# Kernel tuning notes

Measured on AMD Instinct MI355X. Metric: run time of the kernel, lower is better.

The kernel has to match this reference:

```python
import jax, jax.numpy as jnp
import numpy as np

B, C, N = 8, 768, 256
H = 12            # num_heads[0]
D = C // H        # head_dim = 64


def setup_inputs() -> dict:
    key = jax.random.key(0)
    ks = jax.random.split(key, 4)
    s = 0.02
    return {
        "x_ori": jax.random.normal(ks[0], (B, C, N), jnp.float32),
        "cross": jax.random.normal(ks[1], (B, C, N), jnp.float32),
        "W_proj": jax.random.normal(ks[2], (C, C), jnp.float32) * s,
        "b_proj": jnp.zeros((C,), jnp.float32),
        "W_dep": jax.random.normal(ks[3], (C, C), jnp.float32) * s,
        "b_dep": jnp.zeros((C,), jnp.float32),
    }


def reference(x_ori, cross, W_proj, b_proj, W_dep, b_dep):
    # x_ori, cross: [B, C, N] with channel axis factored as (head_dim D, num_heads H)
    Bn, Cn, Nn = x_ori.shape
    Nc = cross.shape[-1]
    scale = D ** (-0.5)

    # 'B (d H) N -> B d (H N)'
    x = x_ori.reshape(Bn, D, H, Nn).reshape(Bn, D, H * Nn)

    # proj over channel axis (1x1 conv): [B, C, Nc]
    cp = jnp.einsum('oc,bcn->bon', W_proj, cross) + b_proj[None, :, None]
    cp = cp.reshape(Bn, D, H, Nc).reshape(Bn, D, H * Nc)      # 'B (d H) Nc -> B d (H Nc)'

    # 'B (d H) Nc -> B (H Nc) d'
    cr = cross.reshape(Bn, D, H, Nc).transpose(0, 2, 3, 1).reshape(Bn, H * Nc, D)

    # raw attention (no softmax in original source)
    atten = jnp.einsum('bdm,bdn->bmn', x, cp) * scale          # [B, H*N, H*Nc]
    out = jnp.einsum('bmn,bnd->bmd', atten, cr)                # [B, H*N, D]

    # 'B (N H) d -> B N (H d)'  (note (num, head) grouping per source)
    out = out.reshape(Bn, Nn, H, D).reshape(Bn, Nn, H * D)

    y = out @ W_dep.T + b_dep                                  # deproj: [B, N, C]
    # skip connection (dropout is identity at eval / drop_ratio=0)
    return x_ori + y.transpose(0, 2, 1)
```

## Files before the change

### kernel.cpp

```cpp
#include <hip/hip_runtime.h>

typedef unsigned short u16;
typedef short bf16x8 __attribute__((ext_vector_type(8)));
typedef float f32x4 __attribute__((ext_vector_type(4)));

#define BB 8
#define CC 768
#define NN 256
#define HH 12
#define DD 64
#define K3 3072
#define BCN 196608
#define SCALE 0.125f
#define LDP 72

__device__ __forceinline__ u16 f2b(float f) {
    union { float f; unsigned int i; } v; v.f = f;
    unsigned int r = v.i + 0x7FFFu + ((v.i >> 16) & 1u);
    return (u16)(r >> 16);
}

__global__ __launch_bounds__(256) void k_prep(
    const float* __restrict__ x, const float* __restrict__ cross, u16* __restrict__ outw)
{
    const int n0 = blockIdx.x * 64;
    const int b  = blockIdx.z;
    const int t  = threadIdx.x;
    __shared__ float T[64][68];
    u16* crT = outw;
    u16* xT  = outw + (size_t)BB * BCN;
    if (blockIdx.y < HH) {
        const int h = blockIdx.y;
        const float* xb = x + b * BCN;
        {
            const int d = t >> 2, fq = t & 3;
            const float* src = xb + (d * HH + h) * NN + n0;
            #pragma unroll
            for (int j = 0; j < 4; ++j) {
                const int nl = (fq + 4 * j) * 4;
                float4 v = *reinterpret_cast<const float4*>(src + nl);
                T[d][nl + 0] = v.x; T[d][nl + 1] = v.y; T[d][nl + 2] = v.z; T[d][nl + 3] = v.w;
            }
        }
        __syncthreads();
        {
            const int nn = t >> 2, dq = t & 3;
            u16* dst = xT + b * BCN + (h * NN + n0 + nn) * DD;
            #pragma unroll
            for (int j = 0; j < 4; ++j) {
                const int d0 = (dq + 4 * j) * 4;
                ushort4 w;
                w.x = f2b(T[d0 + 0][nn]); w.y = f2b(T[d0 + 1][nn]);
                w.z = f2b(T[d0 + 2][nn]); w.w = f2b(T[d0 + 3][nn]);
                *reinterpret_cast<ushort4*>(dst + d0) = w;
            }
        }
    } else {
        const int c0 = (blockIdx.y - HH) * 64;
        const float* crb = cross + b * BCN;
        {
            const int r = t >> 2, fq = t & 3;
            const float* src = crb + (c0 + r) * NN + n0;
            #pragma unroll
            for (int j = 0; j < 4; ++j) {
                const int nl = (fq + 4 * j) * 4;
                float4 v = *reinterpret_cast<const float4*>(src + nl);
                T[r][nl + 0] = v.x; T[r][nl + 1] = v.y; T[r][nl + 2] = v.z; T[r][nl + 3] = v.w;
            }
        }
        __syncthreads();
        {
            const int nn = t >> 2, cq = t & 3;
            u16* dst = crT + b * BCN + (n0 + nn) * CC + c0;
            #pragma unroll
            for (int j = 0; j < 4; ++j) {
                const int cl = (cq + 4 * j) * 4;
                ushort4 w;
                w.x = f2b(T[cl + 0][nn]); w.y = f2b(T[cl + 1][nn]);
                w.z = f2b(T[cl + 2][nn]); w.w = f2b(T[cl + 3][nn]);
                *reinterpret_cast<ushort4*>(dst + cl) = w;
            }
        }
    }
}

__global__ __launch_bounds__(256) void k_proj(
    const float* __restrict__ Wp, const u16* __restrict__ crT_all,
    const float* __restrict__ bp, u16* __restrict__ cp)
{
    const int n0 = blockIdx.x * 64;
    const int o0 = blockIdx.y * 64;
    const int b  = blockIdx.z;
    __shared__ __align__(16) u16 As[64 * LDP];
    __shared__ __align__(16) u16 Bs[64 * LDP];
    const int t = threadIdx.x;
    const int lane = t & 63, wave = t >> 6;
    const int q = lane >> 4, tx = lane & 15;
    const int wm = (wave & 1) * 32, wn = (wave >> 1) * 32;
    const u16* crT = crT_all + b * BCN;
    f32x4 acc[2][2] = {};
    for (int c0 = 0; c0 < CC; c0 += 64) {
        {
            const int r = t >> 2, cq = t & 3;
            const float* src = Wp + (o0 + r) * CC + c0;
            u16* dst = As + r * LDP;
            #pragma unroll
            for (int j = 0; j < 4; ++j) {
                const int cl = (cq + 4 * j) * 4;
                float4 v = *reinterpret_cast<const float4*>(src + cl);
                ushort4 w; w.x = f2b(v.x); w.y = f2b(v.y); w.z = f2b(v.z); w.w = f2b(v.w);
                *reinterpret_cast<ushort4*>(dst + cl) = w;
            }
        }
        {
            const int r = t >> 3, ch = (t & 7) * 8;
            *reinterpret_cast<uint4*>(Bs + r * LDP + ch) =
                *reinterpret_cast<const uint4*>(crT + (n0 + r) * CC + c0 + ch);
            *reinterpret_cast<uint4*>(Bs + (r + 32) * LDP + ch) =
                *reinterpret_cast<const uint4*>(crT + (n0 + r + 32) * CC + c0 + ch);
        }
        __syncthreads();
        #pragma unroll
        for (int kk = 0; kk < 2; ++kk) {
            bf16x8 a0 = *reinterpret_cast<bf16x8*>(As + (wm + tx) * LDP + kk * 32 + q * 8);
            bf16x8 a1 = *reinterpret_cast<bf16x8*>(As + (wm + 16 + tx) * LDP + kk * 32 + q * 8);
            bf16x8 b0 = *reinterpret_cast<bf16x8*>(Bs + (wn + tx) * LDP + kk * 32 + q * 8);
            bf16x8 b1 = *reinterpret_cast<bf16x8*>(Bs + (wn + 16 + tx) * LDP + kk * 32 + q * 8);
            acc[0][0] = __builtin_amdgcn_mfma_f32_16x16x32_bf16(a0, b0, acc[0][0], 0, 0, 0);
            acc[0][1] = __builtin_amdgcn_mfma_f32_16x16x32_bf16(a0, b1, acc[0][1], 0, 0, 0);
            acc[1][0] = __builtin_amdgcn_mfma_f32_16x16x32_bf16(a1, b0, acc[1][0], 0, 0, 0);
            acc[1][1] = __builtin_amdgcn_mfma_f32_16x16x32_bf16(a1, b1, acc[1][1], 0, 0, 0);
        }
        __syncthreads();
    }
    u16* cpb = cp + b * BCN;
    #pragma unroll
    for (int i = 0; i < 2; ++i)
        #pragma unroll
        for (int j = 0; j < 2; ++j)
            #pragma unroll
            for (int r = 0; r < 4; ++r) {
                const int o = o0 + wm + i * 16 + q * 4 + r;
                const int n = n0 + wn + j * 16 + tx;
                cpb[o * NN + n] = f2b(acc[i][j][r] + bp[o]);
            }
}

__global__ __launch_bounds__(256) void k_gram(
    const float* __restrict__ cross, const u16* __restrict__ cp, float* __restrict__ G)
{
    const int kb = blockIdx.x * 64;
    const int b  = blockIdx.y;
    __shared__ __align__(16) u16 As[64 * LDP];
    __shared__ __align__(16) u16 Bs[64 * LDP];
    const int t = threadIdx.x;
    const int lane = t & 63, wave = t >> 6;
    const int q = lane >> 4, tx = lane & 15;
    const int wm = (wave & 1) * 32, wn = (wave >> 1) * 32;
    const float* crb = cross + b * BCN;
    const u16* cpb = cp + b * BCN;
    f32x4 acc[2][2] = {};
    {
        const int r = t >> 2, cq = t & 3;
        const float* src = crb + r * K3 + kb;
        u16* dst = As + r * LDP;
        #pragma unroll
        for (int j = 0; j < 4; ++j) {
            const int cl = (cq + 4 * j) * 4;
            float4 v = *reinterpret_cast<const float4*>(src + cl);
            ushort4 w; w.x = f2b(v.x); w.y = f2b(v.y); w.z = f2b(v.z); w.w = f2b(v.w);
            *reinterpret_cast<ushort4*>(dst + cl) = w;
        }
    }
    {
        const int r = t >> 3, ch = (t & 7) * 8;
        *reinterpret_cast<uint4*>(Bs + r * LDP + ch) =
            *reinterpret_cast<const uint4*>(cpb + r * K3 + kb + ch);
        *reinterpret_cast<uint4*>(Bs + (r + 32) * LDP + ch) =
            *reinterpret_cast<const uint4*>(cpb + (r + 32) * K3 + kb + ch);
    }
    __syncthreads();
    #pragma unroll
    for (int kk = 0; kk < 2; ++kk) {
        bf16x8 a0 = *reinterpret_cast<bf16x8*>(As + (wm + tx) * LDP + kk * 32 + q * 8);
        bf16x8 a1 = *reinterpret_cast<bf16x8*>(As + (wm + 16 + tx) * LDP + kk * 32 + q * 8);
        bf16x8 b0 = *reinterpret_cast<bf16x8*>(Bs + (wn + tx) * LDP + kk * 32 + q * 8);
        bf16x8 b1 = *reinterpret_cast<bf16x8*>(Bs + (wn + 16 + tx) * LDP + kk * 32 + q * 8);
        acc[0][0] = __builtin_amdgcn_mfma_f32_16x16x32_bf16(a0, b0, acc[0][0], 0, 0, 0);
        acc[0][1] = __builtin_amdgcn_mfma_f32_16x16x32_bf16(a0, b1, acc[0][1], 0, 0, 0);
        acc[1][0] = __builtin_amdgcn_mfma_f32_16x16x32_bf16(a1, b0, acc[1][0], 0, 0, 0);
        acc[1][1] = __builtin_amdgcn_mfma_f32_16x16x32_bf16(a1, b1, acc[1][1], 0, 0, 0);
    }
    float* Gb = G + b * 4096;
    #pragma unroll
    for (int i = 0; i < 2; ++i)
        #pragma unroll
        for (int j = 0; j < 2; ++j)
            #pragma unroll
            for (int r = 0; r < 4; ++r) {
                const int dd = wm + i * 16 + q * 4 + r;
                const int d  = wn + j * 16 + tx;
                atomicAdd(Gb + dd * DD + d, acc[i][j][r] * SCALE);
            }
}

__global__ __launch_bounds__(256) void k_xm(
    const u16* __restrict__ xT_all, const float* __restrict__ G, u16* __restrict__ U)
{
    const int m0 = blockIdx.x * 64;
    const int b  = blockIdx.y;
    __shared__ __align__(16) u16 As[64 * LDP];
    __shared__ __align__(16) u16 Bs[64 * LDP];
    const int t = threadIdx.x;
    const int lane = t & 63, wave = t >> 6;
    const int q = lane >> 4, tx = lane & 15;
    const int wm = (wave & 1) * 32, wn = (wave >> 1) * 32;
    const u16* xT = xT_all + b * BCN;
    const float* Gb = G + b * 4096;
    f32x4 acc[2][2] = {};
    {
        const int r = t >> 3, ch = (t & 7) * 8;
        *reinterpret_cast<uint4*>(As + r * LDP + ch) =
            *reinterpret_cast<const uint4*>(xT + (m0 + r) * DD + ch);
        *reinterpret_cast<uint4*>(As + (r + 32) * LDP + ch) =
            *reinterpret_cast<const uint4*>(xT + (m0 + r + 32) * DD + ch);
    }
    {
        const int r = t >> 2, cq = t & 3;
        const float* src = Gb + r * DD;
        u16* dst = Bs + r * LDP;
        #pragma unroll
        for (int j = 0; j < 4; ++j) {
            const int cl = (cq + 4 * j) * 4;
            float4 v = *reinterpret_cast<const float4*>(src + cl);
            ushort4 w; w.x = f2b(v.x); w.y = f2b(v.y); w.z = f2b(v.z); w.w = f2b(v.w);
            *reinterpret_cast<ushort4*>(dst + cl) = w;
        }
    }
    __syncthreads();
    #pragma unroll
    for (int kk = 0; kk < 2; ++kk) {
        bf16x8 a0 = *reinterpret_cast<bf16x8*>(As + (wm + tx) * LDP + kk * 32 + q * 8);
        bf16x8 a1 = *reinterpret_cast<bf16x8*>(As + (wm + 16 + tx) * LDP + kk * 32 + q * 8);
        bf16x8 b0 = *reinterpret_cast<bf16x8*>(Bs + (wn + tx) * LDP + kk * 32 + q * 8);
        bf16x8 b1 = *reinterpret_cast<bf16x8*>(Bs + (wn + 16 + tx) * LDP + kk * 32 + q * 8);
        acc[0][0] = __builtin_amdgcn_mfma_f32_16x16x32_bf16(a0, b0, acc[0][0], 0, 0, 0);
        acc[0][1] = __builtin_amdgcn_mfma_f32_16x16x32_bf16(a0, b1, acc[0][1], 0, 0, 0);
        acc[1][0] = __builtin_amdgcn_mfma_f32_16x16x32_bf16(a1, b0, acc[1][0], 0, 0, 0);
        acc[1][1] = __builtin_amdgcn_mfma_f32_16x16x32_bf16(a1, b1, acc[1][1], 0, 0, 0);
    }
    u16* Ub = U + b * BCN;
    #pragma unroll
    for (int i = 0; i < 2; ++i)
        #pragma unroll
        for (int j = 0; j < 2; ++j)
            #pragma unroll
            for (int r = 0; r < 4; ++r) {
                const int m  = m0 + wm + i * 16 + q * 4 + r;
                const int dd = wn + j * 16 + tx;
                Ub[m * DD + dd] = f2b(acc[i][j][r]);
            }
}

__global__ __launch_bounds__(256) void k_dep(
    const float* __restrict__ Wd, const u16* __restrict__ U,
    const float* __restrict__ bd, const float* __restrict__ x, float* __restrict__ out)
{
    const int n0 = blockIdx.x * 64;
    const int o0 = blockIdx.y * 64;
    const int b  = blockIdx.z;
    __shared__ __align__(16) u16 As[64 * LDP];
    __shared__ __align__(16) u16 Bs[64 * LDP];
    const int t = threadIdx.x;
    const int lane = t & 63, wave = t >> 6;
    const int q = lane >> 4, tx = lane & 15;
    const int wm = (wave & 1) * 32, wn = (wave >> 1) * 32;
    const u16* Ub = U + b * BCN;
    f32x4 acc[2][2] = {};
    for (int c0 = 0; c0 < CC; c0 += 64) {
        {
            const int r = t >> 2, cq = t & 3;
            const float* src = Wd + (o0 + r) * CC + c0;
            u16* dst = As + r * LDP;
            #pragma unroll
            for (int j = 0; j < 4; ++j) {
                const int cl = (cq + 4 * j) * 4;
                float4 v = *reinterpret_cast<const float4*>(src + cl);
                ushort4 w; w.x = f2b(v.x); w.y = f2b(v.y); w.z = f2b(v.z); w.w = f2b(v.w);
                *reinterpret_cast<ushort4*>(dst + cl) = w;
            }
        }
        {
            const int r = t >> 3, ch = (t & 7) * 8;
            *reinterpret_cast<uint4*>(Bs + r * LDP + ch) =
                *reinterpret_cast<const uint4*>(Ub + (n0 + r) * CC + c0 + ch);
            *reinterpret_cast<uint4*>(Bs + (r + 32) * LDP + ch) =
                *reinterpret_cast<const uint4*>(Ub + (n0 + r + 32) * CC + c0 + ch);
        }
        __syncthreads();
        #pragma unroll
        for (int kk = 0; kk < 2; ++kk) {
            bf16x8 a0 = *reinterpret_cast<bf16x8*>(As + (wm + tx) * LDP + kk * 32 + q * 8);
            bf16x8 a1 = *reinterpret_cast<bf16x8*>(As + (wm + 16 + tx) * LDP + kk * 32 + q * 8);
            bf16x8 b0 = *reinterpret_cast<bf16x8*>(Bs + (wn + tx) * LDP + kk * 32 + q * 8);
            bf16x8 b1 = *reinterpret_cast<bf16x8*>(Bs + (wn + 16 + tx) * LDP + kk * 32 + q * 8);
            acc[0][0] = __builtin_amdgcn_mfma_f32_16x16x32_bf16(a0, b0, acc[0][0], 0, 0, 0);
            acc[0][1] = __builtin_amdgcn_mfma_f32_16x16x32_bf16(a0, b1, acc[0][1], 0, 0, 0);
            acc[1][0] = __builtin_amdgcn_mfma_f32_16x16x32_bf16(a1, b0, acc[1][0], 0, 0, 0);
            acc[1][1] = __builtin_amdgcn_mfma_f32_16x16x32_bf16(a1, b1, acc[1][1], 0, 0, 0);
        }
        __syncthreads();
    }
    #pragma unroll
    for (int i = 0; i < 2; ++i)
        #pragma unroll
        for (int j = 0; j < 2; ++j)
            #pragma unroll
            for (int r = 0; r < 4; ++r) {
                const int o = o0 + wm + i * 16 + q * 4 + r;
                const int n = n0 + wn + j * 16 + tx;
                const int idx = b * BCN + o * NN + n;
                out[idx] = acc[i][j][r] + bd[o] + x[idx];
            }
}

extern "C" void kernel_launch(void* const* d_in, const int* in_sizes, int n_in,
                              void* d_out, int out_size, void* d_ws, size_t ws_size,
                              hipStream_t stream) {
    const float* x_ori = (const float*)d_in[0];
    const float* cross = (const float*)d_in[1];
    const float* Wp    = (const float*)d_in[2];
    const float* bp    = (const float*)d_in[3];
    const float* Wd    = (const float*)d_in[4];
    const float* bd    = (const float*)d_in[5];
    float* out = (float*)d_out;

    u16*   cp = (u16*)d_ws;
    u16*   U  = (u16*)d_ws;
    float* G  = (float*)((char*)d_ws + (size_t)BB * BCN * sizeof(u16));
    u16*   prep = (u16*)d_out;
    const u16* crT = prep;
    const u16* xT  = prep + (size_t)BB * BCN;

    hipMemsetAsync(G, 0, (size_t)BB * DD * DD * sizeof(float), stream);
    k_prep<<<dim3(4, 24, BB), 256, 0, stream>>>(x_ori, cross, prep);
    k_proj<<<dim3(4, 12, BB), 256, 0, stream>>>(Wp, crT, bp, cp);
    k_gram<<<dim3(48, BB), 256, 0, stream>>>(cross, cp, G);
    k_xm  <<<dim3(48, BB), 256, 0, stream>>>(xT, G, U);
    k_dep <<<dim3(4, 12, BB), 256, 0, stream>>>(Wd, U, bd, x_ori, out);
}
```

Baseline: 132.9 us.

## Fuse all stages into one cooperative persistent kernel with grid syncs

```diff
diff --git a/kernel.cpp b/kernel.cpp
--- a/kernel.cpp
+++ b/kernel.cpp
@@ -1,4 +1,7 @@
 #include <hip/hip_runtime.h>
+#include <hip/hip_cooperative_groups.h>
+
+namespace cg = cooperative_groups;
 
 typedef unsigned short u16;
 typedef short bf16x8 __attribute__((ext_vector_type(8)));
@@ -13,6 +16,7 @@
 #define BCN 196608
 #define SCALE 0.125f
 #define LDP 72
+#define NBLK 384
 
 __device__ __forceinline__ u16 f2b(float f) {
     union { float f; unsigned int i; } v; v.f = f;
@@ -20,93 +24,171 @@
     return (u16)(r >> 16);
 }
 
-__global__ __launch_bounds__(256) void k_prep(
-    const float* __restrict__ x, const float* __restrict__ cross, u16* __restrict__ outw)
+__global__ __launch_bounds__(256) void k_fused(
+    const float* __restrict__ x, const float* __restrict__ cross,
+    const float* __restrict__ Wp, const float* __restrict__ bp,
+    const float* __restrict__ Wd, const float* __restrict__ bd,
+    char* outbase, char* ws)
 {
-    const int n0 = blockIdx.x * 64;
-    const int b  = blockIdx.z;
-    const int t  = threadIdx.x;
-    __shared__ float T[64][68];
-    u16* crT = outw;
-    u16* xT  = outw + (size_t)BB * BCN;
-    if (blockIdx.y < HH) {
-        const int h = blockIdx.y;
-        const float* xb = x + b * BCN;
-        {
-            const int d = t >> 2, fq = t & 3;
-            const float* src = xb + (d * HH + h) * NN + n0;
-            #pragma unroll
-            for (int j = 0; j < 4; ++j) {
-                const int nl = (fq + 4 * j) * 4;
-                float4 v = *reinterpret_cast<const float4*>(src + nl);
-                T[d][nl + 0] = v.x; T[d][nl + 1] = v.y; T[d][nl + 2] = v.z; T[d][nl + 3] = v.w;
-            }
-        }
-        __syncthreads();
-        {
-            const int nn = t >> 2, dq = t & 3;
-            u16* dst = xT + b * BCN + (h * NN + n0 + nn) * DD;
-            #pragma unroll
-            for (int j = 0; j < 4; ++j) {
-                const int d0 = (dq + 4 * j) * 4;
-                ushort4 w;
-                w.x = f2b(T[d0 + 0][nn]); w.y = f2b(T[d0 + 1][nn]);
-                w.z = f2b(T[d0 + 2][nn]); w.w = f2b(T[d0 + 3][nn]);
-                *reinterpret_cast<ushort4*>(dst + d0) = w;
-            }
-        }
-    } else {
-        const int c0 = (blockIdx.y - HH) * 64;
-        const float* crb = cross + b * BCN;
-        {
-            const int r = t >> 2, fq = t & 3;
-            const float* src = crb + (c0 + r) * NN + n0;
-            #pragma unroll
-            for (int j = 0; j < 4; ++j) {
-                const int nl = (fq + 4 * j) * 4;
-                float4 v = *reinterpret_cast<const float4*>(src + nl);
-                T[r][nl + 0] = v.x; T[r][nl + 1] = v.y; T[r][nl + 2] = v.z; T[r][nl + 3] = v.w;
-            }
-        }
-        __syncthreads();
-        {
-            const int nn = t >> 2, cq = t & 3;
-            u16* dst = crT + b * BCN + (n0 + nn) * CC + c0;
-            #pragma unroll
-            for (int j = 0; j < 4; ++j) {
-                const int cl = (cq + 4 * j) * 4;
-                ushort4 w;
-                w.x = f2b(T[cl + 0][nn]); w.y = f2b(T[cl + 1][nn]);
-                w.z = f2b(T[cl + 2][nn]); w.w = f2b(T[cl + 3][nn]);
-                *reinterpret_cast<ushort4*>(dst + cl) = w;
-            }
-        }
-    }
-}
-
-__global__ __launch_bounds__(256) void k_proj(
-    const float* __restrict__ Wp, const u16* __restrict__ crT_all,
-    const float* __restrict__ bp, u16* __restrict__ cp)
-{
-    const int n0 = blockIdx.x * 64;
-    const int o0 = blockIdx.y * 64;
-    const int b  = blockIdx.z;
-    __shared__ __align__(16) u16 As[64 * LDP];
-    __shared__ __align__(16) u16 Bs[64 * LDP];
+    __shared__ __align__(16) u16 SMEM[2 * 64 * LDP];
+    u16* As = SMEM;
+    u16* Bs = SMEM + 64 * LDP;
+    float (*T)[68] = reinterpret_cast<float(*)[68]>(SMEM);
+
+    float* out = (float*)outbase;
+    u16*   crT = (u16*)outbase;
+    u16*   xT  = crT + (size_t)BB * BCN;
+    u16*   cp  = (u16*)ws;
+    u16*   U   = cp;
+    float* G   = (float*)(ws + (size_t)BB * BCN * sizeof(u16));
+
+    const int blk = blockIdx.x;
     const int t = threadIdx.x;
     const int lane = t & 63, wave = t >> 6;
     const int q = lane >> 4, tx = lane & 15;
     const int wm = (wave & 1) * 32, wn = (wave >> 1) * 32;
-    const u16* crT = crT_all + b * BCN;
-    f32x4 acc[2][2] = {};
-    for (int c0 = 0; c0 < CC; c0 += 64) {
+    cg::grid_group grid = cg::this_grid();
+
+    if (blk < BB) {
+        float* Gb = G + blk * 4096;
+        #pragma unroll
+        for (int j = 0; j < 4; ++j) {
+            float4 z = {0.f, 0.f, 0.f, 0.f};
+            *reinterpret_cast<float4*>(Gb + (t * 4 + j * 1024)) = z;
+        }
+    }
+    #pragma unroll
+    for (int jj = 0; jj < 2; ++jj) {
+        const int j  = blk * 2 + jj;
+        const int n0 = (j & 3) * 64;
+        const int yy = (j >> 2) % 24;
+        const int b  = j / 96;
+        if (yy < HH) {
+            const int h = yy;
+            const float* xb = x + b * BCN;
+            {
+                const int d = t >> 2, fq = t & 3;
+                const float* src = xb + (d * HH + h) * NN + n0;
+                #pragma unroll
+                for (int u = 0; u < 4; ++u) {
+                    const int nl = (fq + 4 * u) * 4;
+                    float4 v = *reinterpret_cast<const float4*>(src + nl);
+                    T[d][nl + 0] = v.x; T[d][nl + 1] = v.y; T[d][nl + 2] = v.z; T[d][nl + 3] = v.w;
+                }
+            }
+            __syncthreads();
+            {
+                const int nn = t >> 2, dq = t & 3;
+                u16* dst = xT + b * BCN + (h * NN + n0 + nn) * DD;
+                #pragma unroll
+                for (int u = 0; u < 4; ++u) {
+                    const int d0 = (dq + 4 * u) * 4;
+                    ushort4 w;
+                    w.x = f2b(T[d0 + 0][nn]); w.y = f2b(T[d0 + 1][nn]);
+                    w.z = f2b(T[d0 + 2][nn]); w.w = f2b(T[d0 + 3][nn]);
+                    *reinterpret_cast<ushort4*>(dst + d0) = w;
+                }
+            }
+        } else {
+            const int c0 = (yy - HH) * 64;
+            const float* crb = cross + b * BCN;
+            {
+                const int r = t >> 2, fq = t & 3;
+                const float* src = crb + (c0 + r) * NN + n0;
+                #pragma unroll
+                for (int u = 0; u < 4; ++u) {
+                    const int nl = (fq + 4 * u) * 4;
+                    float4 v = *reinterpret_cast<const float4*>(src + nl);
+                    T[r][nl + 0] = v.x; T[r][nl + 1] = v.y; T[r][nl + 2] = v.z; T[r][nl + 3] = v.w;
+                }
+            }
+            __syncthreads();
+            {
+                const int nn = t >> 2, cq = t & 3;
+                u16* dst = crT + b * BCN + (n0 + nn) * CC + c0;
+                #pragma unroll
+                for (int u = 0; u < 4; ++u) {
+                    const int cl = (cq + 4 * u) * 4;
+                    ushort4 w;
+                    w.x = f2b(T[cl + 0][nn]); w.y = f2b(T[cl + 1][nn]);
+                    w.z = f2b(T[cl + 2][nn]); w.w = f2b(T[cl + 3][nn]);
+                    *reinterpret_cast<ushort4*>(dst + cl) = w;
+                }
+            }
+        }
+        __syncthreads();
+    }
+
+    grid.sync();
+
+    {
+        const int n0 = (blk & 3) * 64;
+        const int o0 = ((blk >> 2) % 12) * 64;
+        const int b  = blk / 48;
+        const u16* crTb = crT + b * BCN;
+        f32x4 acc[2][2] = {};
+        for (int c0 = 0; c0 < CC; c0 += 64) {
+            {
+                const int r = t >> 2, cq = t & 3;
+                const float* src = Wp + (o0 + r) * CC + c0;
+                u16* dst = As + r * LDP;
+                #pragma unroll
+                for (int u = 0; u < 4; ++u) {
+                    const int cl = (cq + 4 * u) * 4;
+                    float4 v = *reinterpret_cast<const float4*>(src + cl);
+                    ushort4 w; w.x = f2b(v.x); w.y = f2b(v.y); w.z = f2b(v.z); w.w = f2b(v.w);
+                    *reinterpret_cast<ushort4*>(dst + cl) = w;
+                }
+            }
+            {
+                const int r = t >> 3, ch = (t & 7) * 8;
+                *reinterpret_cast<uint4*>(Bs + r * LDP + ch) =
+                    *reinterpret_cast<const uint4*>(crTb + (n0 + r) * CC + c0 + ch);
+                *reinterpret_cast<uint4*>(Bs + (r + 32) * LDP + ch) =
+                    *reinterpret_cast<const uint4*>(crTb + (n0 + r + 32) * CC + c0 + ch);
+            }
+            __syncthreads();
+            #pragma unroll
+            for (int kk = 0; kk < 2; ++kk) {
+                bf16x8 a0 = *reinterpret_cast<bf16x8*>(As + (wm + tx) * LDP + kk * 32 + q * 8);
+                bf16x8 a1 = *reinterpret_cast<bf16x8*>(As + (wm + 16 + tx) * LDP + kk * 32 + q * 8);
+                bf16x8 b0 = *reinterpret_cast<bf16x8*>(Bs + (wn + tx) * LDP + kk * 32 + q * 8);
+                bf16x8 b1 = *reinterpret_cast<bf16x8*>(Bs + (wn + 16 + tx) * LDP + kk * 32 + q * 8);
+                acc[0][0] = __builtin_amdgcn_mfma_f32_16x16x32_bf16(a0, b0, acc[0][0], 0, 0, 0);
+                acc[0][1] = __builtin_amdgcn_mfma_f32_16x16x32_bf16(a0, b1, acc[0][1], 0, 0, 0);
+                acc[1][0] = __builtin_amdgcn_mfma_f32_16x16x32_bf16(a1, b0, acc[1][0], 0, 0, 0);
+                acc[1][1] = __builtin_amdgcn_mfma_f32_16x16x32_bf16(a1, b1, acc[1][1], 0, 0, 0);
+            }
+            __syncthreads();
+        }
+        u16* cpb = cp + b * BCN;
+        #pragma unroll
+        for (int i = 0; i < 2; ++i)
+            #pragma unroll
+            for (int j2 = 0; j2 < 2; ++j2)
+                #pragma unroll
+                for (int r = 0; r < 4; ++r) {
+                    const int o = o0 + wm + i * 16 + q * 4 + r;
+                    const int n = n0 + wn + j2 * 16 + tx;
+                    cpb[o * NN + n] = f2b(acc[i][j2][r] + bp[o]);
+                }
+    }
+
+    grid.sync();
+
+    {
+        const int kb = (blk % 48) * 64;
+        const int b  = blk / 48;
+        const float* crb = cross + b * BCN;
+        const u16* cpb = cp + b * BCN;
+        f32x4 acc[2][2] = {};
         {
             const int r = t >> 2, cq = t & 3;
-            const float* src = Wp + (o0 + r) * CC + c0;
+            const float* src = crb + r * K3 + kb;
             u16* dst = As + r * LDP;
             #pragma unroll
-            for (int j = 0; j < 4; ++j) {
-                const int cl = (cq + 4 * j) * 4;
+            for (int u = 0; u < 4; ++u) {
+                const int cl = (cq + 4 * u) * 4;
                 float4 v = *reinterpret_cast<const float4*>(src + cl);
                 ushort4 w; w.x = f2b(v.x); w.y = f2b(v.y); w.z = f2b(v.z); w.w = f2b(v.w);
                 *reinterpret_cast<ushort4*>(dst + cl) = w;
@@ -115,9 +197,9 @@
         {
             const int r = t >> 3, ch = (t & 7) * 8;
             *reinterpret_cast<uint4*>(Bs + r * LDP + ch) =
-                *reinterpret_cast<const uint4*>(crT + (n0 + r) * CC + c0 + ch);
+                *reinterpret_cast<const uint4*>(cpb + r * K3 + kb + ch);
             *reinterpret_cast<uint4*>(Bs + (r + 32) * LDP + ch) =
-                *reinterpret_cast<const uint4*>(crT + (n0 + r + 32) * CC + c0 + ch);
+                *reinterpret_cast<const uint4*>(cpb + (r + 32) * K3 + kb + ch);
         }
         __syncthreads();
         #pragma unroll
@@ -132,170 +214,45 @@
             acc[1][1] = __builtin_amdgcn_mfma_f32_16x16x32_bf16(a1, b1, acc[1][1], 0, 0, 0);
         }
         __syncthreads();
-    }
-    u16* cpb = cp + b * BCN;
-    #pragma unroll
-    for (int i = 0; i < 2; ++i)
-        #pragma unroll
-        for (int j = 0; j < 2; ++j)
-            #pragma unroll
-            for (int r = 0; r < 4; ++r) {
-                const int o = o0 + wm + i * 16 + q * 4 + r;
-                const int n = n0 + wn + j * 16 + tx;
-                cpb[o * NN + n] = f2b(acc[i][j][r] + bp[o]);
-            }
-}
-
-__global__ __launch_bounds__(256) void k_gram(
-    const float* __restrict__ cross, const u16* __restrict__ cp, float* __restrict__ G)
-{
-    const int kb = blockIdx.x * 64;
-    const int b  = blockIdx.y;
-    __shared__ __align__(16) u16 As[64 * LDP];
-    __shared__ __align__(16) u16 Bs[64 * LDP];
-    const int t = threadIdx.x;
-    const int lane = t & 63, wave = t >> 6;
-    const int q = lane >> 4, tx = lane & 15;
-    const int wm = (wave & 1) * 32, wn = (wave >> 1) * 32;
-    const float* crb = cross + b * BCN;
-    const u16* cpb = cp + b * BCN;
-    f32x4 acc[2][2] = {};
+        float* Gb = G + b * 4096;
+        #pragma unroll
+        for (int i = 0; i < 2; ++i)
+            #pragma unroll
+            for (int j2 = 0; j2 < 2; ++j2)
+                #pragma unroll
+                for (int r = 0; r < 4; ++r) {
+                    const int dd = wm + i * 16 + q * 4 + r;
+                    const int d  = wn + j2 * 16 + tx;
+                    atomicAdd(Gb + dd * DD + d, acc[i][j2][r] * SCALE);
+                }
+    }
+
+    grid.sync();
+
     {
-        const int r = t >> 2, cq = t & 3;
-        const float* src = crb + r * K3 + kb;
-        u16* dst = As + r * LDP;
-        #pragma unroll
-        for (int j = 0; j < 4; ++j) {
-            const int cl = (cq + 4 * j) * 4;
-            float4 v = *reinterpret_cast<const float4*>(src + cl);
-            ushort4 w; w.x = f2b(v.x); w.y = f2b(v.y); w.z = f2b(v.z); w.w = f2b(v.w);
-            *reinterpret_cast<ushort4*>(dst + cl) = w;
-        }
-    }
-    {
-        const int r = t >> 3, ch = (t & 7) * 8;
-        *reinterpret_cast<uint4*>(Bs + r * LDP + ch) =
-            *reinterpret_cast<const uint4*>(cpb + r * K3 + kb + ch);
-        *reinterpret_cast<uint4*>(Bs + (r + 32) * LDP + ch) =
-            *reinterpret_cast<const uint4*>(cpb + (r + 32) * K3 + kb + ch);
-    }
-    __syncthreads();
-    #pragma unroll
-    for (int kk = 0; kk < 2; ++kk) {
-        bf16x8 a0 = *reinterpret_cast<bf16x8*>(As + (wm + tx) * LDP + kk * 32 + q * 8);
-        bf16x8 a1 = *reinterpret_cast<bf16x8*>(As + (wm + 16 + tx) * LDP + kk * 32 + q * 8);
-        bf16x8 b0 = *reinterpret_cast<bf16x8*>(Bs + (wn + tx) * LDP + kk * 32 + q * 8);
-        bf16x8 b1 = *reinterpret_cast<bf16x8*>(Bs + (wn + 16 + tx) * LDP + kk * 32 + q * 8);
-        acc[0][0] = __builtin_amdgcn_mfma_f32_16x16x32_bf16(a0, b0, acc[0][0], 0, 0, 0);
-        acc[0][1] = __builtin_amdgcn_mfma_f32_16x16x32_bf16(a0, b1, acc[0][1], 0, 0, 0);
-        acc[1][0] = __builtin_amdgcn_mfma_f32_16x16x32_bf16(a1, b0, acc[1][0], 0, 0, 0);
-        acc[1][1] = __builtin_amdgcn_mfma_f32_16x16x32_bf16(a1, b1, acc[1][1], 0, 0, 0);
-    }
-    float* Gb = G + b * 4096;
-    #pragma unroll
-    for (int i = 0; i < 2; ++i)
-        #pragma unroll
-        for (int j = 0; j < 2; ++j)
-            #pragma unroll
-            for (int r = 0; r < 4; ++r) {
-                const int dd = wm + i * 16 + q * 4 + r;
-                const int d  = wn + j * 16 + tx;
-                atomicAdd(Gb + dd * DD + d, acc[i][j][r] * SCALE);
-            }
-}
-
-__global__ __launch_bounds__(256) void k_xm(
-    const u16* __restrict__ xT_all, const float* __restrict__ G, u16* __restrict__ U)
-{
-    const int m0 = blockIdx.x * 64;
-    const int b  = blockIdx.y;
-    __shared__ __align__(16) u16 As[64 * LDP];
-    __shared__ __align__(16) u16 Bs[64 * LDP];
-    const int t = threadIdx.x;
-    const int lane = t & 63, wave = t >> 6;
-    const int q = lane >> 4, tx = lane & 15;
-    const int wm = (wave & 1) * 32, wn = (wave >> 1) * 32;
-    const u16* xT = xT_all + b * BCN;
-    const float* Gb = G + b * 4096;
-    f32x4 acc[2][2] = {};
-    {
-        const int r = t >> 3, ch = (t & 7) * 8;
-        *reinterpret_cast<uint4*>(As + r * LDP + ch) =
-            *reinterpret_cast<const uint4*>(xT + (m0 + r) * DD + ch);
-        *reinterpret_cast<uint4*>(As + (r + 32) * LDP + ch) =
-            *reinterpret_cast<const uint4*>(xT + (m0 + r + 32) * DD + ch);
-    }
-    {
-        const int r = t >> 2, cq = t & 3;
-        const float* src = Gb + r * DD;
-        u16* dst = Bs + r * LDP;
-        #pragma unroll
-        for (int j = 0; j < 4; ++j) {
-            const int cl = (cq + 4 * j) * 4;
-            float4 v = *reinterpret_cast<const float4*>(src + cl);
-            ushort4 w; w.x = f2b(v.x); w.y = f2b(v.y); w.z = f2b(v.z); w.w = f2b(v.w);
-            *reinterpret_cast<ushort4*>(dst + cl) = w;
-        }
-    }
-    __syncthreads();
-    #pragma unroll
-    for (int kk = 0; kk < 2; ++kk) {
-        bf16x8 a0 = *reinterpret_cast<bf16x8*>(As + (wm + tx) * LDP + kk * 32 + q * 8);
-        bf16x8 a1 = *reinterpret_cast<bf16x8*>(As + (wm + 16 + tx) * LDP + kk * 32 + q * 8);
-        bf16x8 b0 = *reinterpret_cast<bf16x8*>(Bs + (wn + tx) * LDP + kk * 32 + q * 8);
-        bf16x8 b1 = *reinterpret_cast<bf16x8*>(Bs + (wn + 16 + tx) * LDP + kk * 32 + q * 8);
-        acc[0][0] = __builtin_amdgcn_mfma_f32_16x16x32_bf16(a0, b0, acc[0][0], 0, 0, 0);
-        acc[0][1] = __builtin_amdgcn_mfma_f32_16x16x32_bf16(a0, b1, acc[0][1], 0, 0, 0);
-        acc[1][0] = __builtin_amdgcn_mfma_f32_16x16x32_bf16(a1, b0, acc[1][0], 0, 0, 0);
-        acc[1][1] = __builtin_amdgcn_mfma_f32_16x16x32_bf16(a1, b1, acc[1][1], 0, 0, 0);
-    }
-    u16* Ub = U + b * BCN;
-    #pragma unroll
-    for (int i = 0; i < 2; ++i)
-        #pragma unroll
-        for (int j = 0; j < 2; ++j)
-            #pragma unroll
-            for (int r = 0; r < 4; ++r) {
-                const int m  = m0 + wm + i * 16 + q * 4 + r;
-                const int dd = wn + j * 16 + tx;
-                Ub[m * DD + dd] = f2b(acc[i][j][r]);
-            }
-}
-
-__global__ __launch_bounds__(256) void k_dep(
-    const float* __restrict__ Wd, const u16* __restrict__ U,
-    const float* __restrict__ bd, const float* __restrict__ x, float* __restrict__ out)
-{
-    const int n0 = blockIdx.x * 64;
-    const int o0 = blockIdx.y * 64;
-    const int b  = blockIdx.z;
-    __shared__ __align__(16) u16 As[64 * LDP];
-    __shared__ __align__(16) u16 Bs[64 * LDP];
-    const int t = threadIdx.x;
-    const int lane = t & 63, wave = t >> 6;
-    const int q = lane >> 4, tx = lane & 15;
-    const int wm = (wave & 1) * 32, wn = (wave >> 1) * 32;
-    const u16* Ub = U + b * BCN;
-    f32x4 acc[2][2] = {};
-    for (int c0 = 0; c0 < CC; c0 += 64) {
+        const int m0 = (blk % 48) * 64;
+        const int b  = blk / 48;
+        const u16* xTb = xT + b * BCN;
+        const float* Gb = G + b * 4096;
+        f32x4 acc[2][2] = {};
+        {
+            const int r = t >> 3, ch = (t & 7) * 8;
+            *reinterpret_cast<uint4*>(As + r * LDP + ch) =
+                *reinterpret_cast<const uint4*>(xTb + (m0 + r) * DD + ch);
+            *reinterpret_cast<uint4*>(As + (r + 32) * LDP + ch) =
+                *reinterpret_cast<const uint4*>(xTb + (m0 + r + 32) * DD + ch);
+        }
         {
             const int r = t >> 2, cq = t & 3;
-            const float* src = Wd + (o0 + r) * CC + c0;
-            u16* dst = As + r * LDP;
-            #pragma unroll
-            for (int j = 0; j < 4; ++j) {
-                const int cl = (cq + 4 * j) * 4;
+            const float* src = Gb + r * DD;
+            u16* dst = Bs + r * LDP;
+            #pragma unroll
+            for (int u = 0; u < 4; ++u) {
+                const int cl = (cq + 4 * u) * 4;
                 float4 v = *reinterpret_cast<const float4*>(src + cl);
                 ushort4 w; w.x = f2b(v.x); w.y = f2b(v.y); w.z = f2b(v.z); w.w = f2b(v.w);
                 *reinterpret_cast<ushort4*>(dst + cl) = w;
             }
-        }
-        {
-            const int r = t >> 3, ch = (t & 7) * 8;
-            *reinterpret_cast<uint4*>(Bs + r * LDP + ch) =
-                *reinterpret_cast<const uint4*>(Ub + (n0 + r) * CC + c0 + ch);
-            *reinterpret_cast<uint4*>(Bs + (r + 32) * LDP + ch) =
-                *reinterpret_cast<const uint4*>(Ub + (n0 + r + 32) * CC + c0 + ch);
         }
         __syncthreads();
         #pragma unroll
@@ -310,18 +267,73 @@
             acc[1][1] = __builtin_amdgcn_mfma_f32_16x16x32_bf16(a1, b1, acc[1][1], 0, 0, 0);
         }
         __syncthreads();
-    }
-    #pragma unroll
-    for (int i = 0; i < 2; ++i)
-        #pragma unroll
-        for (int j = 0; j < 2; ++j)
-            #pragma unroll
-            for (int r = 0; r < 4; ++r) {
-                const int o = o0 + wm + i * 16 + q * 4 + r;
-                const int n = n0 + wn + j * 16 + tx;
-                const int idx = b * BCN + o * NN + n;
-                out[idx] = acc[i][j][r] + bd[o] + x[idx];
-            }
+        u16* Ub = U + b * BCN;
+        #pragma unroll
+        for (int i = 0; i < 2; ++i)
+            #pragma unroll
+            for (int j2 = 0; j2 < 2; ++j2)
+                #pragma unroll
+                for (int r = 0; r < 4; ++r) {
+                    const int m  = m0 + wm + i * 16 + q * 4 + r;
+                    const int dd = wn + j2 * 16 + tx;
+                    Ub[m * DD + dd] = f2b(acc[i][j2][r]);
+                }
+    }
+
+    grid.sync();
+
+    {
+        const int n0 = (blk & 3) * 64;
+        const int o0 = ((blk >> 2) % 12) * 64;
+        const int b  = blk / 48;
+        const u16* Ub = U + b * BCN;
+        f32x4 acc[2][2] = {};
+        for (int c0 = 0; c0 < CC; c0 += 64) {
+            {
+                const int r = t >> 2, cq = t & 3;
+                const float* src = Wd + (o0 + r) * CC + c0;
+                u16* dst = As + r * LDP;
+                #pragma unroll
+                for (int u = 0; u < 4; ++u) {
+                    const int cl = (cq + 4 * u) * 4;
+                    float4 v = *reinterpret_cast<const float4*>(src + cl);
+                    ushort4 w; w.x = f2b(v.x); w.y = f2b(v.y); w.z = f2b(v.z); w.w = f2b(v.w);
+                    *reinterpret_cast<ushort4*>(dst + cl) = w;
+                }
+            }
+            {
+                const int r = t >> 3, ch = (t & 7) * 8;
+                *reinterpret_cast<uint4*>(Bs + r * LDP + ch) =
+                    *reinterpret_cast<const uint4*>(Ub + (n0 + r) * CC + c0 + ch);
+                *reinterpret_cast<uint4*>(Bs + (r + 32) * LDP + ch) =
+                    *reinterpret_cast<const uint4*>(Ub + (n0 + r + 32) * CC + c0 + ch);
+            }
+            __syncthreads();
+            #pragma unroll
+            for (int kk = 0; kk < 2; ++kk) {
+                bf16x8 a0 = *reinterpret_cast<bf16x8*>(As + (wm + tx) * LDP + kk * 32 + q * 8);
+                bf16x8 a1 = *reinterpret_cast<bf16x8*>(As + (wm + 16 + tx) * LDP + kk * 32 + q * 8);
+                bf16x8 b0 = *reinterpret_cast<bf16x8*>(Bs + (wn + tx) * LDP + kk * 32 + q * 8);
+                bf16x8 b1 = *reinterpret_cast<bf16x8*>(Bs + (wn + 16 + tx) * LDP + kk * 32 + q * 8);
+                acc[0][0] = __builtin_amdgcn_mfma_f32_16x16x32_bf16(a0, b0, acc[0][0], 0, 0, 0);
+                acc[0][1] = __builtin_amdgcn_mfma_f32_16x16x32_bf16(a0, b1, acc[0][1], 0, 0, 0);
+                acc[1][0] = __builtin_amdgcn_mfma_f32_16x16x32_bf16(a1, b0, acc[1][0], 0, 0, 0);
+                acc[1][1] = __builtin_amdgcn_mfma_f32_16x16x32_bf16(a1, b1, acc[1][1], 0, 0, 0);
+            }
+            __syncthreads();
+        }
+        #pragma unroll
+        for (int i = 0; i < 2; ++i)
+            #pragma unroll
+            for (int j2 = 0; j2 < 2; ++j2)
+                #pragma unroll
+                for (int r = 0; r < 4; ++r) {
+                    const int o = o0 + wm + i * 16 + q * 4 + r;
+                    const int n = n0 + wn + j2 * 16 + tx;
+                    const int idx = b * BCN + o * NN + n;
+                    out[idx] = acc[i][j2][r] + bd[o] + x[idx];
+                }
+    }
 }
 
 extern "C" void kernel_launch(void* const* d_in, const int* in_sizes, int n_in,
@@ -333,19 +345,11 @@
     const float* bp    = (const float*)d_in[3];
     const float* Wd    = (const float*)d_in[4];
     const float* bd    = (const float*)d_in[5];
-    float* out = (float*)d_out;
-
-    u16*   cp = (u16*)d_ws;
-    u16*   U  = (u16*)d_ws;
-    float* G  = (float*)((char*)d_ws + (size_t)BB * BCN * sizeof(u16));
-    u16*   prep = (u16*)d_out;
-    const u16* crT = prep;
-    const u16* xT  = prep + (size_t)BB * BCN;
-
-    hipMemsetAsync(G, 0, (size_t)BB * DD * DD * sizeof(float), stream);
-    k_prep<<<dim3(4, 24, BB), 256, 0, stream>>>(x_ori, cross, prep);
-    k_proj<<<dim3(4, 12, BB), 256, 0, stream>>>(Wp, crT, bp, cp);
-    k_gram<<<dim3(48, BB), 256, 0, stream>>>(cross, cp, G);
-    k_xm  <<<dim3(48, BB), 256, 0, stream>>>(xT, G, U);
-    k_dep <<<dim3(4, 12, BB), 256, 0, stream>>>(Wd, U, bd, x_ori, out);
+    char* outbase = (char*)d_out;
+    char* ws      = (char*)d_ws;
+
+    void* args[] = { (void*)&x_ori, (void*)&cross, (void*)&Wp, (void*)&bp,
+                     (void*)&Wd, (void*)&bd, (void*)&outbase, (void*)&ws };
+    hipLaunchCooperativeKernel((const void*)k_fused, dim3(NBLK), dim3(256),
+                               args, 0, stream);
 }
```

After: 317.9 us. 139% more time.

## Fold transpose/bf16 prep into proj and xm kernels, drop memset

Applied to the files above, without the earlier changes.

```diff
diff --git a/kernel.cpp b/kernel.cpp
--- a/kernel.cpp
+++ b/kernel.cpp
@@ -20,84 +20,30 @@
     return (u16)(r >> 16);
 }
 
-__global__ __launch_bounds__(256) void k_prep(
-    const float* __restrict__ x, const float* __restrict__ cross, u16* __restrict__ outw)
+__global__ __launch_bounds__(256) void k_proj(
+    const float* __restrict__ Wp, const float* __restrict__ cross,
+    const float* __restrict__ bp, u16* __restrict__ cp, float* __restrict__ G)
 {
-    const int n0 = blockIdx.x * 64;
-    const int b  = blockIdx.z;
-    const int t  = threadIdx.x;
-    __shared__ float T[64][68];
-    u16* crT = outw;
-    u16* xT  = outw + (size_t)BB * BCN;
-    if (blockIdx.y < HH) {
-        const int h = blockIdx.y;
-        const float* xb = x + b * BCN;
-        {
-            const int d = t >> 2, fq = t & 3;
-            const float* src = xb + (d * HH + h) * NN + n0;
-            #pragma unroll
-            for (int j = 0; j < 4; ++j) {
-                const int nl = (fq + 4 * j) * 4;
-                float4 v = *reinterpret_cast<const float4*>(src + nl);
-                T[d][nl + 0] = v.x; T[d][nl + 1] = v.y; T[d][nl + 2] = v.z; T[d][nl + 3] = v.w;
-            }
-        }
-        __syncthreads();
-        {
-            const int nn = t >> 2, dq = t & 3;
-            u16* dst = xT + b * BCN + (h * NN + n0 + nn) * DD;
-            #pragma unroll
-            for (int j = 0; j < 4; ++j) {
-                const int d0 = (dq + 4 * j) * 4;
-                ushort4 w;
-                w.x = f2b(T[d0 + 0][nn]); w.y = f2b(T[d0 + 1][nn]);
-                w.z = f2b(T[d0 + 2][nn]); w.w = f2b(T[d0 + 3][nn]);
-                *reinterpret_cast<ushort4*>(dst + d0) = w;
-            }
-        }
-    } else {
-        const int c0 = (blockIdx.y - HH) * 64;
-        const float* crb = cross + b * BCN;
-        {
-            const int r = t >> 2, fq = t & 3;
-            const float* src = crb + (c0 + r) * NN + n0;
-            #pragma unroll
-            for (int j = 0; j < 4; ++j) {
-                const int nl = (fq + 4 * j) * 4;
-                float4 v = *reinterpret_cast<const float4*>(src + nl);
-                T[r][nl + 0] = v.x; T[r][nl + 1] = v.y; T[r][nl + 2] = v.z; T[r][nl + 3] = v.w;
-            }
-        }
-        __syncthreads();
-        {
-            const int nn = t >> 2, cq = t & 3;
-            u16* dst = crT + b * BCN + (n0 + nn) * CC + c0;
-            #pragma unroll
-            for (int j = 0; j < 4; ++j) {
-                const int cl = (cq + 4 * j) * 4;
-                ushort4 w;
-                w.x = f2b(T[cl + 0][nn]); w.y = f2b(T[cl + 1][nn]);
-                w.z = f2b(T[cl + 2][nn]); w.w = f2b(T[cl + 3][nn]);
-                *reinterpret_cast<ushort4*>(dst + cl) = w;
-            }
-        }
-    }
-}
-
-__global__ __launch_bounds__(256) void k_proj(
-    const float* __restrict__ Wp, const u16* __restrict__ crT_all,
-    const float* __restrict__ bp, u16* __restrict__ cp)
-{
+    __shared__ __align__(16) u16 As[64 * LDP];
+    __shared__ __align__(16) u16 Bs[64 * LDP];
+    __shared__ __align__(16) float T[64][68];
     const int n0 = blockIdx.x * 64;
     const int o0 = blockIdx.y * 64;
     const int b  = blockIdx.z;
-    __shared__ __align__(16) u16 As[64 * LDP];
-    __shared__ __align__(16) u16 Bs[64 * LDP];
     const int t = threadIdx.x;
     const int lane = t & 63, wave = t >> 6;
     const int q = lane >> 4, tx = lane & 15;
     const int wm = (wave & 1) * 32, wn = (wave >> 1) * 32;
-    const u16* crT = crT_all + b * BCN;
+
+    if (blockIdx.x == 0 && blockIdx.y == 0) {
+        float4 z = {0.f, 0.f, 0.f, 0.f};
+        float* Gb = G + b * 4096;
+        #pragma unroll
+        for (int j = 0; j < 4; ++j)
+            *reinterpret_cast<float4*>(Gb + t * 4 + j * 1024) = z;
+    }
+
+    const float* crb = cross + b * BCN;
     f32x4 acc[2][2] = {};
     for (int c0 = 0; c0 < CC; c0 += 64) {
         {
@@ -105,19 +51,35 @@
             const float* src = Wp + (o0 + r) * CC + c0;
             u16* dst = As + r * LDP;
             #pragma unroll
-            for (int j = 0; j < 4; ++j) {
-                const int cl = (cq + 4 * j) * 4;
+            for (int u = 0; u < 4; ++u) {
+                const int cl = (cq + 4 * u) * 4;
                 float4 v = *reinterpret_cast<const float4*>(src + cl);
                 ushort4 w; w.x = f2b(v.x); w.y = f2b(v.y); w.z = f2b(v.z); w.w = f2b(v.w);
                 *reinterpret_cast<ushort4*>(dst + cl) = w;
             }
         }
         {
-            const int r = t >> 3, ch = (t & 7) * 8;
-            *reinterpret_cast<uint4*>(Bs + r * LDP + ch) =
-                *reinterpret_cast<const uint4*>(crT + (n0 + r) * CC + c0 + ch);
-            *reinterpret_cast<uint4*>(Bs + (r + 32) * LDP + ch) =
-                *reinterpret_cast<const uint4*>(crT + (n0 + r + 32) * CC + c0 + ch);
+            const int r = t >> 2, fq = t & 3;
+            const float* src = crb + (c0 + r) * NN + n0;
+            #pragma unroll
+            for (int u = 0; u < 4; ++u) {
+                const int nl = (fq + 4 * u) * 4;
+                float4 v = *reinterpret_cast<const float4*>(src + nl);
+                T[r][nl + 0] = v.x; T[r][nl + 1] = v.y; T[r][nl + 2] = v.z; T[r][nl + 3] = v.w;
+            }
+        }
+        __syncthreads();
+        {
+            const int nn = t >> 2, cq = t & 3;
+            u16* dst = Bs + nn * LDP;
+            #pragma unroll
+            for (int u = 0; u < 4; ++u) {
+                const int c4 = (cq + 4 * u) * 4;
+                ushort4 w;
+                w.x = f2b(T[c4 + 0][nn]); w.y = f2b(T[c4 + 1][nn]);
+                w.z = f2b(T[c4 + 2][nn]); w.w = f2b(T[c4 + 3][nn]);
+                *reinterpret_cast<ushort4*>(dst + c4) = w;
+            }
         }
         __syncthreads();
         #pragma unroll
@@ -149,10 +111,10 @@
 __global__ __launch_bounds__(256) void k_gram(
     const float* __restrict__ cross, const u16* __restrict__ cp, float* __restrict__ G)
 {
+    __shared__ __align__(16) u16 As[64 * LDP];
+    __shared__ __align__(16) u16 Bs[64 * LDP];
     const int kb = blockIdx.x * 64;
     const int b  = blockIdx.y;
-    __shared__ __align__(16) u16 As[64 * LDP];
-    __shared__ __align__(16) u16 Bs[64 * LDP];
     const int t = threadIdx.x;
     const int lane = t & 63, wave = t >> 6;
     const int q = lane >> 4, tx = lane & 15;
@@ -165,8 +127,8 @@
         const float* src = crb + r * K3 + kb;
         u16* dst = As + r * LDP;
         #pragma unroll
-        for (int j = 0; j < 4; ++j) {
-            const int cl = (cq + 4 * j) * 4;
+        for (int u = 0; u < 4; ++u) {
+            const int cl = (cq + 4 * u) * 4;
             float4 v = *reinterpret_cast<const float4*>(src + cl);
             ushort4 w; w.x = f2b(v.x); w.y = f2b(v.y); w.z = f2b(v.z); w.w = f2b(v.w);
             *reinterpret_cast<ushort4*>(dst + cl) = w;
@@ -205,36 +167,55 @@
 }
 
 __global__ __launch_bounds__(256) void k_xm(
-    const u16* __restrict__ xT_all, const float* __restrict__ G, u16* __restrict__ U)
+    const float* __restrict__ x, const float* __restrict__ G, u16* __restrict__ U)
 {
+    __shared__ __align__(16) u16 As[64 * LDP];
+    __shared__ __align__(16) u16 Bs[64 * LDP];
+    __shared__ __align__(16) float T[64][68];
     const int m0 = blockIdx.x * 64;
     const int b  = blockIdx.y;
-    __shared__ __align__(16) u16 As[64 * LDP];
-    __shared__ __align__(16) u16 Bs[64 * LDP];
+    const int h   = m0 >> 8;
+    const int nn0 = m0 & 255;
     const int t = threadIdx.x;
     const int lane = t & 63, wave = t >> 6;
     const int q = lane >> 4, tx = lane & 15;
     const int wm = (wave & 1) * 32, wn = (wave >> 1) * 32;
-    const u16* xT = xT_all + b * BCN;
+    const float* xb = x + b * BCN;
     const float* Gb = G + b * 4096;
     f32x4 acc[2][2] = {};
     {
-        const int r = t >> 3, ch = (t & 7) * 8;
-        *reinterpret_cast<uint4*>(As + r * LDP + ch) =
-            *reinterpret_cast<const uint4*>(xT + (m0 + r) * DD + ch);
-        *reinterpret_cast<uint4*>(As + (r + 32) * LDP + ch) =
-            *reinterpret_cast<const uint4*>(xT + (m0 + r + 32) * DD + ch);
+        const int d = t >> 2, fq = t & 3;
+        const float* src = xb + (d * HH + h) * NN + nn0;
+        #pragma unroll
+        for (int u = 0; u < 4; ++u) {
+            const int nl = (fq + 4 * u) * 4;
+            float4 v = *reinterpret_cast<const float4*>(src + nl);
+            T[d][nl + 0] = v.x; T[d][nl + 1] = v.y; T[d][nl + 2] = v.z; T[d][nl + 3] = v.w;
+        }
     }
     {
         const int r = t >> 2, cq = t & 3;
         const float* src = Gb + r * DD;
         u16* dst = Bs + r * LDP;
         #pragma unroll
-        for (int j = 0; j < 4; ++j) {
-            const int cl = (cq + 4 * j) * 4;
+        for (int u = 0; u < 4; ++u) {
+            const int cl = (cq + 4 * u) * 4;
             float4 v = *reinterpret_cast<const float4*>(src + cl);
             ushort4 w; w.x = f2b(v.x); w.y = f2b(v.y); w.z = f2b(v.z); w.w = f2b(v.w);
             *reinterpret_cast<ushort4*>(dst + cl) = w;
+        }
+    }
+    __syncthreads();
+    {
+        const int nn = t >> 2, dq = t & 3;
+        u16* dst = As + nn * LDP;
+        #pragma unroll
+        for (int u = 0; u < 4; ++u) {
+            const int d4 = (dq + 4 * u) * 4;
+            ushort4 w;
+            w.x = f2b(T[d4 + 0][nn]); w.y = f2b(T[d4 + 1][nn]);
+            w.z = f2b(T[d4 + 2][nn]); w.w = f2b(T[d4 + 3][nn]);
+            *reinterpret_cast<ushort4*>(dst + d4) = w;
         }
     }
     __syncthreads();
@@ -266,11 +247,11 @@
     const float* __restrict__ Wd, const u16* __restrict__ U,
     const float* __restrict__ bd, const float* __restrict__ x, float* __restrict__ out)
 {
+    __shared__ __align__(16) u16 As[64 * LDP];
+    __shared__ __align__(16) u16 Bs[64 * LDP];
     const int n0 = blockIdx.x * 64;
     const int o0 = blockIdx.y * 64;
     const int b  = blockIdx.z;
-    __shared__ __align__(16) u16 As[64 * LDP];
-    __shared__ __align__(16) u16 Bs[64 * LDP];
     const int t = threadIdx.x;
     const int lane = t & 63, wave = t >> 6;
     const int q = lane >> 4, tx = lane & 15;
@@ -283,8 +264,8 @@
             const float* src = Wd + (o0 + r) * CC + c0;
             u16* dst = As + r * LDP;
             #pragma unroll
-            for (int j = 0; j < 4; ++j) {
-                const int cl = (cq + 4 * j) * 4;
+            for (int u = 0; u < 4; ++u) {
+                const int cl = (cq + 4 * u) * 4;
                 float4 v = *reinterpret_cast<const float4*>(src + cl);
                 ushort4 w; w.x = f2b(v.x); w.y = f2b(v.y); w.z = f2b(v.z); w.w = f2b(v.w);
                 *reinterpret_cast<ushort4*>(dst + cl) = w;
@@ -338,14 +319,9 @@
     u16*   cp = (u16*)d_ws;
     u16*   U  = (u16*)d_ws;
     float* G  = (float*)((char*)d_ws + (size_t)BB * BCN * sizeof(u16));
-    u16*   prep = (u16*)d_out;
-    const u16* crT = prep;
-    const u16* xT  = prep + (size_t)BB * BCN;
-
-    hipMemsetAsync(G, 0, (size_t)BB * DD * DD * sizeof(float), stream);
-    k_prep<<<dim3(4, 24, BB), 256, 0, stream>>>(x_ori, cross, prep);
-    k_proj<<<dim3(4, 12, BB), 256, 0, stream>>>(Wp, crT, bp, cp);
+
+    k_proj<<<dim3(4, 12, BB), 256, 0, stream>>>(Wp, cross, bp, cp, G);
     k_gram<<<dim3(48, BB), 256, 0, stream>>>(cross, cp, G);
-    k_xm  <<<dim3(48, BB), 256, 0, stream>>>(xT, G, U);
+    k_xm  <<<dim3(48, BB), 256, 0, stream>>>(x_ori, G, U);
     k_dep <<<dim3(4, 12, BB), 256, 0, stream>>>(Wd, U, bd, x_ori, out);
 }
```

Result: faster. 124.8 us, median of 2 (-6.1%).
